# Kernel optimization log

Hardware: AMD Instinct MI355X
Metric: run time of the kernel (lower is better)

The kernel has to match this reference:

```python
import jax, jax.numpy as jnp
import numpy as np

B, S, D = 2, 2048, 1024
H, DK = 16, 64  # num_heads, key_dim (value_dim defaults to key_dim)


def setup_inputs() -> dict:
    key = jax.random.key(0)
    ks = jax.random.split(key, 11)
    init = lambda k, shape, fan_in: jax.random.uniform(
        k, shape, jnp.float32, -1.0, 1.0) * (1.0 / np.sqrt(fan_in))
    return {
        "query": jax.random.normal(ks[0], (B, S, D), jnp.float32),
        "key": jax.random.normal(ks[1], (B, S, D), jnp.float32),
        "value": jax.random.normal(ks[2], (B, S, D), jnp.float32),
        "Wq": init(ks[3], (D, H, DK), D),
        "bq": jnp.zeros((H, DK), jnp.float32),
        "Wk": init(ks[4], (D, H, DK), D),
        "bk": jnp.zeros((H, DK), jnp.float32),
        "Wv": init(ks[5], (D, H, DK), D),
        "bv": jnp.zeros((H, DK), jnp.float32),
        "Wo": init(ks[6], (H, DK, D), H * DK),
        "bo": jnp.zeros((D,), jnp.float32),
    }


def reference(query, key, value, Wq, bq, Wk, bk, Wv, bv, Wo, bo):
    # QKV projections: abc,cde->abde (EinsumDense with bias on (H, DK))
    q = jnp.einsum("bsd,dhk->bshk", query, Wq) + bq  # [B,S,H,DK]
    k = jnp.einsum("bsd,dhk->bshk", key, Wk) + bk
    v = jnp.einsum("bsd,dhk->bshk", value, Wv) + bv
    # Keras scales the query before the dot product
    q = q * (1.0 / jnp.sqrt(jnp.asarray(DK, q.dtype)))
    # aecd,abcd->acbe : [B,H,Sq,Sk]
    scores = jnp.einsum("bqhk,bshk->bhqs", q, k)
    probs = jax.nn.softmax(scores, axis=-1)
    # acbe,aecd->abcd : [B,Sq,H,DK]
    attn = jnp.einsum("bhqs,bshk->bqhk", probs, v)
    # output projection: abcd,cde->abe
    out = jnp.einsum("bqhk,hkd->bqd", attn, Wo) + bo  # [B,S,D]
    return out
```

## Files before the change

### kernel.cpp

```cpp
#include <hip/hip_runtime.h>
#include <hip/hip_bf16.h>
#include <stdint.h>
#include <stddef.h>


typedef __bf16 bf16;
typedef __attribute__((ext_vector_type(4))) bf16 bf16x4;
typedef __attribute__((ext_vector_type(8))) bf16 bf16x8;
typedef __attribute__((ext_vector_type(4))) float f32x4;
typedef __attribute__((ext_vector_type(16))) float f32x16;
typedef __attribute__((ext_vector_type(2))) unsigned int uint2v;

#define DEVINL static __device__ __forceinline__

DEVINL void gload_lds16(const void* g, void* l) {
  __builtin_amdgcn_global_load_lds(
      (const __attribute__((address_space(1))) void*)g,
      (__attribute__((address_space(3))) void*)l, 16, 0, 0);
}

DEVINL f32x4 mfma16(bf16x8 a, bf16x8 b, f32x4 c) {
  return __builtin_amdgcn_mfma_f32_16x16x32_bf16(a, b, c, 0, 0, 0);
}
DEVINL f32x16 mfma32(bf16x8 a, bf16x8 b, f32x16 c) {
  return __builtin_amdgcn_mfma_f32_32x32x16_bf16(a, b, c, 0, 0, 0);
}
DEVINL float fexp2(float x) {
  float r;
  asm("v_exp_f32 %0, %1" : "=v"(r) : "v"(x));
  return r;
}
DEVINL unsigned pack2(float lo, float hi) {
  union { bf16 h[2]; unsigned u; } t;
  t.h[0] = (bf16)lo; t.h[1] = (bf16)hi;
  return t.u;
}
DEVINL bf16x8 mk8(unsigned a, unsigned b, unsigned c, unsigned d) {
  union { unsigned u[4]; bf16x8 v; } t;
  t.u[0] = a; t.u[1] = b; t.u[2] = c; t.u[3] = d;
  return t.v;
}

__global__ __launch_bounds__(256) void prep_kernel(
    const float* __restrict__ q, const float* __restrict__ k,
    const float* __restrict__ v,
    const float* __restrict__ w0, const float* __restrict__ w1,
    const float* __restrict__ w2, const float* __restrict__ w3,
    bf16* __restrict__ Abf, bf16* __restrict__ Wt) {
  __shared__ float tile[64 * 65];
  int bx = blockIdx.x;
  if (bx < 6144) {
    int z = bx >> 11, blk = bx & 2047;
    const float* src = (z == 0) ? q : (z == 1) ? k : v;
    size_t off = ((size_t)blk * 256 + threadIdx.x) * 8;
    f32x4 a = *(const f32x4*)(src + off);
    f32x4 b = *(const f32x4*)(src + off + 4);
    bf16x8 h;
#pragma unroll
    for (int j = 0; j < 4; ++j) { h[j] = (bf16)a[j]; h[4 + j] = (bf16)b[j]; }
    *(bf16x8*)(Abf + (size_t)z * 4194304 + off) = h;
  } else {
    int tb = bx - 6144;
    int t = tb >> 8;
    tb &= 255;
    const float* w = (t == 0) ? w0 : (t == 1) ? w1 : (t == 2) ? w2 : w3;
    bf16* o = Wt + (size_t)t * 1024 * 1024;
    int k0 = (tb >> 4) * 64, n0 = (tb & 15) * 64;
    int c = threadIdx.x & 63, r0 = threadIdx.x >> 6;
    for (int r = r0; r < 64; r += 4)
      tile[r * 65 + c] = w[(size_t)(k0 + r) * 1024 + n0 + c];
    __syncthreads();
    for (int r = r0; r < 64; r += 4)
      o[(size_t)(n0 + r) * 1024 + k0 + c] = (bf16)tile[c * 65 + r];
  }
}

__global__ __launch_bounds__(256) void gemm_qkv(
    const bf16* __restrict__ Abf, const bf16* __restrict__ Wt,
    const float* __restrict__ bq, const float* __restrict__ bk,
    const float* __restrict__ bv,
    bf16* __restrict__ outQ, bf16* __restrict__ outK, bf16* __restrict__ Vt) {
  int z = blockIdx.z;
  const bf16* A    = Abf + (size_t)z * 4194304;
  const bf16* Wz   = Wt + (size_t)z * 1024 * 1024;
  const float* bia = (z == 0) ? bq : (z == 1) ? bk : bv;
  float scale      = (z == 0) ? 0.18033688011112042f : 1.0f;

  __shared__ bf16 As[2][128 * 32];
  __shared__ bf16 Bs[2][128 * 32];

  int m0 = blockIdx.x * 128, n0 = blockIdx.y * 128;
  int tid = threadIdx.x, w = tid >> 6, l = tid & 63;
  int wm = (w >> 1) * 64, wn = (w & 1) * 64;
  int c16 = l & 15, g = l >> 4;
  int rsw = (c16 >> 1) & 3;

  int brow0 = (w * 2 + 0) * 16 + (l >> 2);
  int brow1 = (w * 2 + 1) * 16 + (l >> 2);
  int bk0 = ((l & 3) ^ ((brow0 >> 1) & 3)) * 8;
  int bk1 = ((l & 3) ^ ((brow1 >> 1) & 3)) * 8;

  f32x4 acc[4][4] = {};

#define STAGE_QKV(buf, kt)                                                   \
  do {                                                                       \
    gload_lds16(A + (size_t)(m0 + brow0) * 1024 + (kt) + bk0,                \
                (char*)As[buf] + (w * 2 + 0) * 1024 + l * 16);               \
    gload_lds16(A + (size_t)(m0 + brow1) * 1024 + (kt) + bk1,                \
                (char*)As[buf] + (w * 2 + 1) * 1024 + l * 16);               \
    gload_lds16(Wz + (size_t)(n0 + brow0) * 1024 + (kt) + bk0,               \
                (char*)Bs[buf] + (w * 2 + 0) * 1024 + l * 16);               \
    gload_lds16(Wz + (size_t)(n0 + brow1) * 1024 + (kt) + bk1,               \
                (char*)Bs[buf] + (w * 2 + 1) * 1024 + l * 16);               \
  } while (0)

  STAGE_QKV(0, 0);
  __syncthreads();

  int cur = 0;
  for (int kt = 0; kt < 1024; kt += 32) {
    if (kt < 992) STAGE_QKV(cur ^ 1, kt + 32);
    bf16x8 af[4], bfr[4];
#pragma unroll
    for (int mt = 0; mt < 4; ++mt)
      af[mt] = *(const bf16x8*)&As[cur][(wm + mt * 16 + c16) * 32 + ((g ^ rsw) * 8)];
#pragma unroll
    for (int nt = 0; nt < 4; ++nt)
      bfr[nt] = *(const bf16x8*)&Bs[cur][(wn + nt * 16 + c16) * 32 + ((g ^ rsw) * 8)];
#pragma unroll
    for (int mt = 0; mt < 4; ++mt)
#pragma unroll
      for (int nt = 0; nt < 4; ++nt)
        acc[mt][nt] = mfma16(af[mt], bfr[nt], acc[mt][nt]);
    __syncthreads();
    cur ^= 1;
  }
#undef STAGE_QKV

  if (z < 2) {
    bf16* Cout = (z == 0) ? outQ : outK;
#pragma unroll
    for (int mt = 0; mt < 4; ++mt)
#pragma unroll
      for (int nt = 0; nt < 4; ++nt) {
        int n = n0 + wn + nt * 16 + c16;
        float bb = bia[n];
#pragma unroll
        for (int r = 0; r < 4; ++r) {
          int m = m0 + wm + mt * 16 + g * 4 + r;
          Cout[(size_t)m * 1024 + n] = (bf16)((acc[mt][nt][r] + bb) * scale);
        }
      }
  } else {
#pragma unroll
    for (int mt = 0; mt < 4; ++mt)
#pragma unroll
      for (int nt = 0; nt < 4; ++nt) {
        int n = n0 + wn + nt * 16 + c16;
        float bb = bia[n];
        int m = m0 + wm + mt * 16 + g * 4;
        int b = m >> 11, s = m & 2047;
        bf16x4 v;
#pragma unroll
        for (int r = 0; r < 4; ++r) v[r] = (bf16)(acc[mt][nt][r] + bb);
        *(bf16x4*)&Vt[((size_t)(b * 16 + (n >> 6)) * 64 + (n & 63)) * 2048 + s] = v;
      }
  }
}

__global__ __launch_bounds__(256, 2) void flash_kernel(
    const bf16* __restrict__ Qp, const bf16* __restrict__ Kp,
    const bf16* __restrict__ Vt, bf16* __restrict__ AO) {
  __shared__ __align__(16) bf16 Ks[4][64 * 64];
  __shared__ __align__(16) bf16 Vs[4][64 * 64];

  int orig = blockIdx.x;
  int wg = (orig & 7) * 64 + (orig >> 3);
  int bh = wg >> 4, qb = wg & 15;
  int b = bh >> 4, h = bh & 15;
  int tid = threadIdx.x, w = tid >> 6, l = tid & 63;
  int lo5 = l & 31, g = l >> 5;
  int q0 = qb * 128 + w * 32;

  const bf16* qptr = Qp + (size_t)(b * 2048 + q0 + lo5) * 1024 + h * 64 + g * 8;
  bf16x8 qf0 = *(const bf16x8*)(qptr + 0);
  bf16x8 qf1 = *(const bf16x8*)(qptr + 16);
  bf16x8 qf2 = *(const bf16x8*)(qptr + 32);
  bf16x8 qf3 = *(const bf16x8*)(qptr + 48);

  const bf16* kbase = Kp + (size_t)(b * 2048) * 1024 + h * 64;
  const bf16* vbase = Vt + (size_t)bh * 64 * 2048;

  int u0 = w * 64 + l;
  int u1 = (4 + w) * 64 + l;
  int r0s = u0 >> 3, c0s = (u0 & 7) ^ (r0s & 7);
  int r1s = u1 >> 3, c1s = (u1 & 7) ^ (r1s & 7);

#define STAGE(buf, s0)                                                          \
  do {                                                                          \
    gload_lds16(kbase + (size_t)((s0) + r0s) * 1024 + c0s * 8,                  \
                (bf16*)Ks[buf] + u0 * 8);                                       \
    gload_lds16(kbase + (size_t)((s0) + r1s) * 1024 + c1s * 8,                  \
                (bf16*)Ks[buf] + u1 * 8);                                       \
    gload_lds16(vbase + (size_t)r0s * 2048 + (s0) + c0s * 8,                    \
                (bf16*)Vs[buf] + u0 * 8);                                       \
    gload_lds16(vbase + (size_t)r1s * 2048 + (s0) + c1s * 8,                    \
                (bf16*)Vs[buf] + u1 * 8);                                       \
  } while (0)

#define LDSK(cp, nt, kt) \
  (*(const bf16x8*)&cp[(((nt)*32 + lo5) << 6) + (((((kt)*2 + g)) ^ (lo5 & 7)) << 3)])
#define LDSV(cp, dt, st) \
  (*(const bf16x8*)&cp[(((dt)*32 + lo5) << 6) + (((((st)*2 + g)) ^ (lo5 & 7)) << 3)])

#define QK(d0, d1, kc)                                                          \
  do {                                                                          \
    __builtin_amdgcn_s_setprio(1);                                              \
    d0 = z16; d1 = z16;                                                         \
    d0 = mfma32(LDSK(kc, 0, 0), qf0, d0);                                       \
    d0 = mfma32(LDSK(kc, 0, 1), qf1, d0);                                       \
    d0 = mfma32(LDSK(kc, 0, 2), qf2, d0);                                       \
    d0 = mfma32(LDSK(kc, 0, 3), qf3, d0);                                       \
    d1 = mfma32(LDSK(kc, 1, 0), qf0, d1);                                       \
    d1 = mfma32(LDSK(kc, 1, 1), qf1, d1);                                       \
    d1 = mfma32(LDSK(kc, 1, 2), qf2, d1);                                       \
    d1 = mfma32(LDSK(kc, 1, 3), qf3, d1);                                       \
    __builtin_amdgcn_s_setprio(0);                                              \
  } while (0)

#define SOFTMAX(sv, sw)                                                         \
  do {                                                                          \
    float p[16];                                                                \
    _Pragma("unroll") for (int r = 0; r < 16; ++r) p[r] = fexp2(sv[r]);         \
    ps0 += p[0] + p[4] + p[8] + p[12];                                          \
    ps1 += p[1] + p[5] + p[9] + p[13];                                          \
    ps2 += p[2] + p[6] + p[10] + p[14];                                         \
    ps3 += p[3] + p[7] + p[11] + p[15];                                         \
    unsigned pw0 = pack2(p[0], p[1]), pw1 = pack2(p[2], p[3]);                  \
    unsigned pw2 = pack2(p[4], p[5]), pw3 = pack2(p[6], p[7]);                  \
    unsigned pw4 = pack2(p[8], p[9]), pw5 = pack2(p[10], p[11]);                \
    unsigned pw6 = pack2(p[12], p[13]), pw7 = pack2(p[14], p[15]);              \
    uint2v a02 = __builtin_amdgcn_permlane32_swap(pw0, pw2, false, false);      \
    uint2v a13 = __builtin_amdgcn_permlane32_swap(pw1, pw3, false, false);      \
    uint2v a46 = __builtin_amdgcn_permlane32_swap(pw4, pw6, false, false);      \
    uint2v a57 = __builtin_amdgcn_permlane32_swap(pw5, pw7, false, false);      \
    pa0 = mk8(a02.x, a13.x, a02.y, a13.y);                                      \
    pa1 = mk8(a46.x, a57.x, a46.y, a57.y);                                      \
    _Pragma("unroll") for (int r = 0; r < 16; ++r) p[r] = fexp2(sw[r]);         \
    ps0 += p[0] + p[4] + p[8] + p[12];                                          \
    ps1 += p[1] + p[5] + p[9] + p[13];                                          \
    ps2 += p[2] + p[6] + p[10] + p[14];                                         \
    ps3 += p[3] + p[7] + p[11] + p[15];                                         \
    pw0 = pack2(p[0], p[1]); pw1 = pack2(p[2], p[3]);                           \
    pw2 = pack2(p[4], p[5]); pw3 = pack2(p[6], p[7]);                           \
    pw4 = pack2(p[8], p[9]); pw5 = pack2(p[10], p[11]);                         \
    pw6 = pack2(p[12], p[13]); pw7 = pack2(p[14], p[15]);                       \
    a02 = __builtin_amdgcn_permlane32_swap(pw0, pw2, false, false);             \
    a13 = __builtin_amdgcn_permlane32_swap(pw1, pw3, false, false);             \
    a46 = __builtin_amdgcn_permlane32_swap(pw4, pw6, false, false);             \
    a57 = __builtin_amdgcn_permlane32_swap(pw5, pw7, false, false);             \
    pb0 = mk8(a02.x, a13.x, a02.y, a13.y);                                      \
    pb1 = mk8(a46.x, a57.x, a46.y, a57.y);                                      \
  } while (0)

#define PV(vc)                                                                  \
  do {                                                                          \
    __builtin_amdgcn_s_setprio(1);                                              \
    o0 = mfma32(pa0, LDSV(vc, 0, 0), o0);                                       \
    o1 = mfma32(pa0, LDSV(vc, 1, 0), o1);                                       \
    o0 = mfma32(pa1, LDSV(vc, 0, 1), o0);                                       \
    o1 = mfma32(pa1, LDSV(vc, 1, 1), o1);                                       \
    o0 = mfma32(pb0, LDSV(vc, 0, 2), o0);                                       \
    o1 = mfma32(pb0, LDSV(vc, 1, 2), o1);                                       \
    o0 = mfma32(pb1, LDSV(vc, 0, 3), o0);                                       \
    o1 = mfma32(pb1, LDSV(vc, 1, 3), o1);                                       \
    __builtin_amdgcn_s_setprio(0);                                              \
  } while (0)

  const f32x16 z16 = {};
  f32x16 o0 = z16, o1 = z16;
  f32x16 sA0, sA1, sB0, sB1;
  bf16x8 pa0, pa1, pb0, pb1;
  float ps0 = 0.f, ps1 = 0.f, ps2 = 0.f, ps3 = 0.f;

  STAGE(0, 0);
  STAGE(1, 64);
  asm volatile("s_waitcnt vmcnt(6)" ::: "memory");
  __builtin_amdgcn_s_barrier();
  __builtin_amdgcn_sched_barrier(0);
  QK(sA0, sA1, Ks[0]);

  for (int t = 0; t < 32; t += 2) {
    if (t < 30) {
      STAGE((t + 2) & 3, (t + 2) * 64);
      asm volatile("s_waitcnt vmcnt(6)" ::: "memory");
    } else {
      asm volatile("s_waitcnt vmcnt(2)" ::: "memory");
    }
    __builtin_amdgcn_s_barrier();
    __builtin_amdgcn_sched_barrier(0);
    QK(sB0, sB1, Ks[(t + 1) & 3]);
    SOFTMAX(sA0, sA1);
    PV(Vs[t & 3]);

    if (t < 29) {
      STAGE((t + 3) & 3, (t + 3) * 64);
      asm volatile("s_waitcnt vmcnt(6)" ::: "memory");
    } else {
      asm volatile("s_waitcnt vmcnt(0)" ::: "memory");
    }
    __builtin_amdgcn_s_barrier();
    __builtin_amdgcn_sched_barrier(0);
    if (t < 30) QK(sA0, sA1, Ks[(t + 2) & 3]);
    SOFTMAX(sB0, sB1);
    PV(Vs[(t + 1) & 3]);
  }
#undef STAGE
#undef LDSK
#undef LDSV
#undef QK
#undef SOFTMAX
#undef PV

  float plsum = (ps0 + ps1) + (ps2 + ps3);
  float tot = plsum + __shfl_xor(plsum, 32);

#pragma unroll
  for (int r = 0; r < 16; ++r) {
    int qr = (r & 3) + 8 * (r >> 2) + 4 * g;
    float inv = 1.0f / __shfl(tot, qr);
    bf16* op = AO + (size_t)(b * 2048 + q0 + qr) * 1024 + h * 64 + lo5;
    op[0]  = (bf16)(o0[r] * inv);
    op[32] = (bf16)(o1[r] * inv);
  }
}

__global__ __launch_bounds__(256) void gemm_o(
    const bf16* __restrict__ A, const bf16* __restrict__ Wt3,
    const float* __restrict__ bo, float* __restrict__ C) {
  __shared__ bf16 As[2][64 * 32];
  __shared__ bf16 Bs[2][128 * 32];
  int m0 = blockIdx.x * 64, n0 = blockIdx.y * 128;
  int tid = threadIdx.x, w = tid >> 6, l = tid & 63;
  int wm = (w >> 1) * 32, wn = (w & 1) * 64;
  int c16 = l & 15, g = l >> 4;
  int rsw = (c16 >> 1) & 3;

  int arow = tid >> 2, akc = tid & 3;
  int asrc = (akc ^ ((arow >> 1) & 3)) * 8;
  int brow0 = (w * 2 + 0) * 16 + (l >> 2);
  int brow1 = (w * 2 + 1) * 16 + (l >> 2);
  int bk0 = ((l & 3) ^ ((brow0 >> 1) & 3)) * 8;
  int bk1 = ((l & 3) ^ ((brow1 >> 1) & 3)) * 8;

  f32x4 acc[2][4] = {};

#define STAGE_O(buf, kt)                                                     \
  do {                                                                       \
    gload_lds16(A + (size_t)(m0 + arow) * 1024 + (kt) + asrc,                \
                (char*)As[buf] + tid * 16);                                  \
    gload_lds16(Wt3 + (size_t)(n0 + brow0) * 1024 + (kt) + bk0,              \
                (char*)Bs[buf] + (w * 2 + 0) * 1024 + l * 16);               \
    gload_lds16(Wt3 + (size_t)(n0 + brow1) * 1024 + (kt) + bk1,              \
                (char*)Bs[buf] + (w * 2 + 1) * 1024 + l * 16);               \
  } while (0)

  STAGE_O(0, 0);
  __syncthreads();

  int cur = 0;
  for (int kt = 0; kt < 1024; kt += 32) {
    if (kt < 992) STAGE_O(cur ^ 1, kt + 32);
    bf16x8 af[2], bfr[4];
#pragma unroll
    for (int mt = 0; mt < 2; ++mt)
      af[mt] = *(const bf16x8*)&As[cur][(wm + mt * 16 + c16) * 32 + ((g ^ rsw) * 8)];
#pragma unroll
    for (int nt = 0; nt < 4; ++nt)
      bfr[nt] = *(const bf16x8*)&Bs[cur][(wn + nt * 16 + c16) * 32 + ((g ^ rsw) * 8)];
#pragma unroll
    for (int mt = 0; mt < 2; ++mt)
#pragma unroll
      for (int nt = 0; nt < 4; ++nt)
        acc[mt][nt] = mfma16(af[mt], bfr[nt], acc[mt][nt]);
    __syncthreads();
    cur ^= 1;
  }
#undef STAGE_O

#pragma unroll
  for (int mt = 0; mt < 2; ++mt)
#pragma unroll
    for (int nt = 0; nt < 4; ++nt) {
      int n = n0 + wn + nt * 16 + c16;
      float bb = bo[n];
#pragma unroll
      for (int r = 0; r < 4; ++r) {
        int m = m0 + wm + mt * 16 + g * 4 + r;
        C[(size_t)m * 1024 + n] = acc[mt][nt][r] + bb;
      }
    }
}

extern "C" void kernel_launch(void* const* d_in, const int* in_sizes, int n_in,
                              void* d_out, int out_size, void* d_ws, size_t ws_size,
                              hipStream_t stream) {
  const float* query = (const float*)d_in[0];
  const float* key_  = (const float*)d_in[1];
  const float* value = (const float*)d_in[2];
  const float* Wq = (const float*)d_in[3];
  const float* bq = (const float*)d_in[4];
  const float* Wk = (const float*)d_in[5];
  const float* bk = (const float*)d_in[6];
  const float* Wv = (const float*)d_in[7];
  const float* bv = (const float*)d_in[8];
  const float* Wo = (const float*)d_in[9];
  const float* bo = (const float*)d_in[10];
  float* out = (float*)d_out;

  char* ws = (char*)d_ws;
  const size_t MB = 1024 * 1024;
  bf16* Wt  = (bf16*)(ws);
  bf16* Abf = (bf16*)(ws + 8 * MB);
  bf16* Qp  = (bf16*)(ws + 32 * MB);
  bf16* Kp  = (bf16*)(ws + 40 * MB);
  bf16* Vt  = (bf16*)(ws + 48 * MB);
  bf16* AO  = (bf16*)(ws + 8 * MB);

  prep_kernel<<<dim3(7168), dim3(256), 0, stream>>>(query, key_, value,
                                                    Wq, Wk, Wv, Wo, Abf, Wt);
  gemm_qkv<<<dim3(32, 8, 3), dim3(256), 0, stream>>>(Abf, Wt, bq, bk, bv,
                                                     Qp, Kp, Vt);
  flash_kernel<<<dim3(512), dim3(256), 0, stream>>>(Qp, Kp, Vt, AO);
  gemm_o<<<dim3(64, 8), dim3(256), 0, stream>>>(AO, Wt + (size_t)3 * 1024 * 1024, bo, out);
}
```

Before: 127.4 us.

## Deepen flash attention software pipeline so PV lags softmax by two tiles

Restructures the flash attention main loop so each tile's P·V product runs two stages behind its QK, overlapping one tile's softmax with an earlier tile's PV. Two sets of packed probability registers alternate between stages. The prologue and epilogue are unrolled explicitly, and launch bounds drop from 2 to 1 waves-per-SIMD target to leave room for the extra registers. This trades occupancy for more instruction-level overlap between MFMA and exp/permute work. It also risks an LDS buffer reuse hazard: a V buffer can be restaged while other waves may still be reading it.

New measurement: 145.7 us. +14.4%, slower.

```diff
diff --git a/kernel.cpp b/kernel.cpp
--- a/kernel.cpp
+++ b/kernel.cpp
@@ -168,7 +168,7 @@
   }
 }
 
-__global__ __launch_bounds__(256, 2) void flash_kernel(
+__global__ __launch_bounds__(256, 1) void flash_kernel(
     const bf16* __restrict__ Qp, const bf16* __restrict__ Kp,
     const bf16* __restrict__ Vt, bf16* __restrict__ AO) {
   __shared__ __align__(16) bf16 Ks[4][64 * 64];
@@ -228,7 +228,7 @@
     __builtin_amdgcn_s_setprio(0);                                              \
   } while (0)
 
-#define SOFTMAX(sv, sw)                                                         \
+#define SOFTMAX(sv, sw, ta0, ta1, tb0, tb1)                                     \
   do {                                                                          \
     float p[16];                                                                \
     _Pragma("unroll") for (int r = 0; r < 16; ++r) p[r] = fexp2(sv[r]);         \
@@ -244,8 +244,8 @@
     uint2v a13 = __builtin_amdgcn_permlane32_swap(pw1, pw3, false, false);      \
     uint2v a46 = __builtin_amdgcn_permlane32_swap(pw4, pw6, false, false);      \
     uint2v a57 = __builtin_amdgcn_permlane32_swap(pw5, pw7, false, false);      \
-    pa0 = mk8(a02.x, a13.x, a02.y, a13.y);                                      \
-    pa1 = mk8(a46.x, a57.x, a46.y, a57.y);                                      \
+    ta0 = mk8(a02.x, a13.x, a02.y, a13.y);                                      \
+    ta1 = mk8(a46.x, a57.x, a46.y, a57.y);                                      \
     _Pragma("unroll") for (int r = 0; r < 16; ++r) p[r] = fexp2(sw[r]);         \
     ps0 += p[0] + p[4] + p[8] + p[12];                                          \
     ps1 += p[1] + p[5] + p[9] + p[13];                                          \
@@ -259,68 +259,79 @@
     a13 = __builtin_amdgcn_permlane32_swap(pw1, pw3, false, false);             \
     a46 = __builtin_amdgcn_permlane32_swap(pw4, pw6, false, false);             \
     a57 = __builtin_amdgcn_permlane32_swap(pw5, pw7, false, false);             \
-    pb0 = mk8(a02.x, a13.x, a02.y, a13.y);                                      \
-    pb1 = mk8(a46.x, a57.x, a46.y, a57.y);                                      \
-  } while (0)
-
-#define PV(vc)                                                                  \
+    tb0 = mk8(a02.x, a13.x, a02.y, a13.y);                                      \
+    tb1 = mk8(a46.x, a57.x, a46.y, a57.y);                                      \
+  } while (0)
+
+#define PV(vc, a0, a1, b0, b1)                                                  \
   do {                                                                          \
     __builtin_amdgcn_s_setprio(1);                                              \
-    o0 = mfma32(pa0, LDSV(vc, 0, 0), o0);                                       \
-    o1 = mfma32(pa0, LDSV(vc, 1, 0), o1);                                       \
-    o0 = mfma32(pa1, LDSV(vc, 0, 1), o0);                                       \
-    o1 = mfma32(pa1, LDSV(vc, 1, 1), o1);                                       \
-    o0 = mfma32(pb0, LDSV(vc, 0, 2), o0);                                       \
-    o1 = mfma32(pb0, LDSV(vc, 1, 2), o1);                                       \
-    o0 = mfma32(pb1, LDSV(vc, 0, 3), o0);                                       \
-    o1 = mfma32(pb1, LDSV(vc, 1, 3), o1);                                       \
+    o0 = mfma32(a0, LDSV(vc, 0, 0), o0);                                        \
+    o1 = mfma32(a0, LDSV(vc, 1, 0), o1);                                        \
+    o0 = mfma32(a1, LDSV(vc, 0, 1), o0);                                        \
+    o1 = mfma32(a1, LDSV(vc, 1, 1), o1);                                        \
+    o0 = mfma32(b0, LDSV(vc, 0, 2), o0);                                        \
+    o1 = mfma32(b0, LDSV(vc, 1, 2), o1);                                        \
+    o0 = mfma32(b1, LDSV(vc, 0, 3), o0);                                        \
+    o1 = mfma32(b1, LDSV(vc, 1, 3), o1);                                        \
     __builtin_amdgcn_s_setprio(0);                                              \
+  } while (0)
+
+#define WAITBAR(n)                                                              \
+  do {                                                                          \
+    asm volatile("s_waitcnt vmcnt(" #n ")" ::: "memory");                       \
+    __builtin_amdgcn_s_barrier();                                               \
+    __builtin_amdgcn_sched_barrier(0);                                          \
   } while (0)
 
   const f32x16 z16 = {};
   f32x16 o0 = z16, o1 = z16;
   f32x16 sA0, sA1, sB0, sB1;
-  bf16x8 pa0, pa1, pb0, pb1;
+  bf16x8 pAa0, pAa1, pAb0, pAb1;
+  bf16x8 pBa0, pBa1, pBb0, pBb1;
   float ps0 = 0.f, ps1 = 0.f, ps2 = 0.f, ps3 = 0.f;
 
   STAGE(0, 0);
   STAGE(1, 64);
-  asm volatile("s_waitcnt vmcnt(6)" ::: "memory");
-  __builtin_amdgcn_s_barrier();
-  __builtin_amdgcn_sched_barrier(0);
+  WAITBAR(6);
   QK(sA0, sA1, Ks[0]);
-
-  for (int t = 0; t < 32; t += 2) {
-    if (t < 30) {
-      STAGE((t + 2) & 3, (t + 2) * 64);
-      asm volatile("s_waitcnt vmcnt(6)" ::: "memory");
-    } else {
-      asm volatile("s_waitcnt vmcnt(2)" ::: "memory");
-    }
-    __builtin_amdgcn_s_barrier();
-    __builtin_amdgcn_sched_barrier(0);
+  STAGE(2, 128);
+  WAITBAR(6);
+  QK(sB0, sB1, Ks[1]);
+  SOFTMAX(sA0, sA1, pAa0, pAa1, pAb0, pAb1);
+
+  for (int t = 2; t < 30; t += 2) {
+    STAGE((t + 1) & 3, (t + 1) * 64);
+    WAITBAR(6);
+    QK(sA0, sA1, Ks[t & 3]);
+    SOFTMAX(sB0, sB1, pBa0, pBa1, pBb0, pBb1);
+    PV(Vs[(t - 2) & 3], pAa0, pAa1, pAb0, pAb1);
+    STAGE((t + 2) & 3, (t + 2) * 64);
+    WAITBAR(6);
     QK(sB0, sB1, Ks[(t + 1) & 3]);
-    SOFTMAX(sA0, sA1);
-    PV(Vs[t & 3]);
-
-    if (t < 29) {
-      STAGE((t + 3) & 3, (t + 3) * 64);
-      asm volatile("s_waitcnt vmcnt(6)" ::: "memory");
-    } else {
-      asm volatile("s_waitcnt vmcnt(0)" ::: "memory");
-    }
-    __builtin_amdgcn_s_barrier();
-    __builtin_amdgcn_sched_barrier(0);
-    if (t < 30) QK(sA0, sA1, Ks[(t + 2) & 3]);
-    SOFTMAX(sB0, sB1);
-    PV(Vs[(t + 1) & 3]);
-  }
+    SOFTMAX(sA0, sA1, pAa0, pAa1, pAb0, pAb1);
+    PV(Vs[(t - 1) & 3], pBa0, pBa1, pBb0, pBb1);
+  }
+  STAGE(31 & 3, 31 * 64);
+  WAITBAR(6);
+  QK(sA0, sA1, Ks[30 & 3]);
+  SOFTMAX(sB0, sB1, pBa0, pBa1, pBb0, pBb1);
+  PV(Vs[28 & 3], pAa0, pAa1, pAb0, pAb1);
+  WAITBAR(2);
+  QK(sB0, sB1, Ks[31 & 3]);
+  SOFTMAX(sA0, sA1, pAa0, pAa1, pAb0, pAb1);
+  PV(Vs[29 & 3], pBa0, pBa1, pBb0, pBb1);
+  WAITBAR(0);
+  SOFTMAX(sB0, sB1, pBa0, pBa1, pBb0, pBb1);
+  PV(Vs[30 & 3], pAa0, pAa1, pAb0, pAb1);
+  PV(Vs[31 & 3], pBa0, pBa1, pBb0, pBb1);
 #undef STAGE
 #undef LDSK
 #undef LDSV
 #undef QK
 #undef SOFTMAX
 #undef PV
+#undef WAITBAR
 
   float plsum = (ps0 + ps1) + (ps2 + ps3);
   float tot = plsum + __shfl_xor(plsum, 32);
```
